# Kernel tuning notes

Measured on AMD Instinct MI355X. Metric: run time of the kernel, lower is better.

Reference implementation:

```python
import jax, jax.numpy as jnp
from jax import lax
import numpy as np

B, N, NPOINT, NSAMPLE, RADIUS = 8, 16384, 1024, 32, 0.4
C_IN = 64


def fps(xyz, npoint):
    """Furthest point sampling. xyz: (B, N, 3) -> (B, npoint) int32 indices.
    Matches the CUDA kernel: start from index 0, iteratively pick argmax of
    the running min-distance to the selected set."""
    Bb, Nn, _ = xyz.shape

    def step(carry, _):
        min_d, last = carry
        p = jnp.take_along_axis(xyz, last[:, None, None], axis=1)  # (B,1,3)
        d = jnp.sum((xyz - p) ** 2, axis=-1)                       # (B,N)
        min_d = jnp.minimum(min_d, d)
        nxt = jnp.argmax(min_d, axis=1).astype(jnp.int32)
        return (min_d, nxt), nxt

    idx0 = jnp.zeros((Bb,), jnp.int32)
    min_d0 = jnp.full((Bb, Nn), jnp.inf, xyz.dtype)
    _, rest = lax.scan(step, (min_d0, idx0), None, length=npoint - 1)  # (npoint-1, B)
    return jnp.transpose(jnp.concatenate([idx0[None, :], rest], axis=0))  # (B, npoint)


def ball_query(xyz, new_xyz, radius, nsample):
    """xyz: (B,N,3), new_xyz: (B,P,3) -> (B,P,nsample) int32 indices.
    First nsample in-radius indices (ascending), short balls padded with the
    first found index (the centroid itself is always in-radius)."""
    Nn = xyz.shape[1]
    d2 = jnp.sum((new_xyz[:, :, None, :] - xyz[:, None, :, :]) ** 2, axis=-1)  # (B,P,N)
    ar = jnp.arange(Nn, dtype=jnp.int32)
    key = jnp.where(d2 <= radius * radius, ar, Nn)  # out-of-ball -> sentinel N
    neg_top, _ = lax.top_k(-key, nsample)           # nsample smallest keys
    gidx = -neg_top                                  # (B,P,nsample)
    return jnp.where(gidx == Nn, gidx[..., :1], gidx)


def setup_inputs() -> dict:
    key = jax.random.key(0)
    ks = jax.random.split(key, 8)
    return {
        "xyz": jax.random.normal(ks[0], (B, N, 3), jnp.float32),
        "features": jax.random.normal(ks[1], (B, C_IN, N), jnp.float32),
        "W1": jax.random.normal(ks[2], (64, 3 + C_IN), jnp.float32) * 0.05,
        "b1": jax.random.normal(ks[3], (64,), jnp.float32) * 0.05,
        "W2": jax.random.normal(ks[4], (64, 64), jnp.float32) * 0.05,
        "b2": jax.random.normal(ks[5], (64,), jnp.float32) * 0.05,
        "W3": jax.random.normal(ks[6], (128, 64), jnp.float32) * 0.05,
        "b3": jax.random.normal(ks[7], (128,), jnp.float32) * 0.05,
    }


def reference(xyz, features, W1, b1, W2, b2, W3, b3):
    Bb = xyz.shape[0]
    idx = fps(xyz, NPOINT)                                         # (B,P)
    new_xyz = jnp.take_along_axis(xyz, idx[:, :, None], axis=1)    # (B,P,3)

    gidx = ball_query(xyz, new_xyz, RADIUS, NSAMPLE)               # (B,P,S)
    bi = jnp.arange(Bb)[:, None, None]
    grouped_xyz = xyz[bi, gidx] - new_xyz[:, :, None, :]           # (B,P,S,3) relative coords
    feats_t = jnp.transpose(features, (0, 2, 1))                   # (B,N,C)
    grouped_feats = feats_t[bi, gidx]                              # (B,P,S,C)
    h = jnp.concatenate([grouped_xyz, grouped_feats], axis=-1)     # (B,P,S,3+C)

    # shared per-point MLP (1x1 convs) + ReLU
    h = jax.nn.relu(jnp.einsum('bpsc,oc->bpso', h, W1) + b1)
    h = jax.nn.relu(jnp.einsum('bpsc,oc->bpso', h, W2) + b2)
    h = jax.nn.relu(jnp.einsum('bpsc,oc->bpso', h, W3) + b3)

    pooled = jnp.max(h, axis=2)                                    # (B,P,128) max over nsample
    new_features = jnp.transpose(pooled, (0, 2, 1))                # (B,128,P)
    return new_xyz, new_features
```

## Files before the change

### kernel.cpp

```cpp
#include <hip/hip_runtime.h>

#define R2 0.16f

typedef float f32x2 __attribute__((ext_vector_type(2)));

__device__ __forceinline__ float sqd(float x, float y, float z,
                                     float px, float py, float pz) {
  float dx = __fsub_rn(x, px);
  float dy = __fsub_rn(y, py);
  float dz = __fsub_rn(z, pz);
  return __fadd_rn(__fadd_rn(__fmul_rn(dx, dx), __fmul_rn(dy, dy)),
                   __fmul_rn(dz, dz));
}

__device__ __forceinline__ float wave64_max_dpp(float x) {
#define DPP_STEP(CTRL)                                                      \
  {                                                                         \
    int t_ = __builtin_amdgcn_update_dpp(__float_as_int(x),                 \
                                         __float_as_int(x), CTRL, 0xf, 0xf, \
                                         false);                            \
    x = fmaxf(x, __int_as_float(t_));                                       \
  }
  DPP_STEP(0x111) DPP_STEP(0x112) DPP_STEP(0x114)
  DPP_STEP(0x118) DPP_STEP(0x142) DPP_STEP(0x143)
#undef DPP_STEP
  return x;
}
__device__ __forceinline__ float wave64_min_dpp_f32(float x) {
#define DPP_STEP(CTRL)                                                      \
  {                                                                         \
    int t_ = __builtin_amdgcn_update_dpp(__float_as_int(x),                 \
                                         __float_as_int(x), CTRL, 0xf, 0xf, \
                                         false);                            \
    x = fminf(x, __int_as_float(t_));                                       \
  }
  DPP_STEP(0x111) DPP_STEP(0x112) DPP_STEP(0x114)
  DPP_STEP(0x118) DPP_STEP(0x142) DPP_STEP(0x143)
#undef DPP_STEP
  return x;
}
__device__ __forceinline__ unsigned wave64_min_dpp_u32(unsigned x) {
#define DPP_STEP(CTRL)                                                      \
  {                                                                         \
    unsigned t_ = (unsigned)__builtin_amdgcn_update_dpp(                    \
        (int)x, (int)x, CTRL, 0xf, 0xf, false);                             \
    x = (t_ < x) ? t_ : x;                                                  \
  }
  DPP_STEP(0x111) DPP_STEP(0x112) DPP_STEP(0x114)
  DPP_STEP(0x118) DPP_STEP(0x142) DPP_STEP(0x143)
#undef DPP_STEP
  return x;
}

__global__ __launch_bounds__(256) void zero_hist(unsigned* __restrict__ h) {
  h[blockIdx.x * 256 + threadIdx.x] = 0u;
}

__global__ __launch_bounds__(256) void hist_kernel(const float* __restrict__ xyz,
                                                   unsigned* __restrict__ hist,
                                                   unsigned* __restrict__ rank,
                                                   unsigned* __restrict__ cid) {
  int t = blockIdx.x * 256 + threadIdx.x;
  int b = t >> 14;
  const float* p = xyz + (size_t)t * 3;
  int cx = (int)floorf(p[0] + 4.0f);
  int cy = (int)floorf(p[1] + 4.0f);
  int cz = (int)floorf(p[2] + 4.0f);
  cx = min(max(cx, 0), 7);
  cy = min(max(cy, 0), 7);
  cz = min(max(cz, 0), 7);
  unsigned c = (unsigned)(cx | (cy << 3) | (cz << 6));
  unsigned r = atomicAdd(&hist[(b << 9) + c], 1u);
  rank[t] = r;
  cid[t] = c;
}

__global__ __launch_bounds__(512) void scan_kernel(const unsigned* __restrict__ hist,
                                                   unsigned* __restrict__ starts) {
  __shared__ unsigned a[512];
  int b = blockIdx.x, t = threadIdx.x;
  unsigned h = hist[(b << 9) + t];
  a[t] = h;
  __syncthreads();
  for (int s = 1; s < 512; s <<= 1) {
    unsigned v = (t >= s) ? a[t - s] : 0u;
    __syncthreads();
    a[t] += v;
    __syncthreads();
  }
  starts[(b << 9) + t] = a[t] - h;
}

__global__ __launch_bounds__(256) void scatter_kernel(
    const float* __restrict__ xyz, const unsigned* __restrict__ starts,
    const unsigned* __restrict__ rank, const unsigned* __restrict__ cid,
    float* __restrict__ xs2, float* __restrict__ ys2, float* __restrict__ zs2,
    unsigned* __restrict__ oi2) {
  int t = blockIdx.x * 256 + threadIdx.x;
  int b = t >> 14, n = t & 16383;
  unsigned pos = starts[(b << 9) + cid[t]] + rank[t];
  const float* p = xyz + (size_t)t * 3;
  size_t o = ((size_t)b << 14) + pos;
  xs2[o] = p[0];
  ys2[o] = p[1];
  zs2[o] = p[2];
  oi2[o] = (unsigned)n;
}

__global__ __launch_bounds__(1024) void fps_kernel(
    const float* __restrict__ xyz, const float* __restrict__ xs,
    const float* __restrict__ ys, const float* __restrict__ zs,
    const unsigned* __restrict__ oi, int* __restrict__ idx_out,
    float* __restrict__ newxyz_out, const float* __restrict__ feats,
    float* __restrict__ featsT) {
#pragma clang fp contract(off)
  extern __shared__ float4 xylds[];
  __shared__ unsigned long long s_gkey[3];
  __shared__ float s_cd[3][3][16];
  int tid = threadIdx.x;
  if (blockIdx.x >= 8) {
    int sub = tid >> 8, t = tid & 255;
    int tileid = (blockIdx.x - 8) * 4 + sub;
    int b = tileid >> 8;
    int n0 = (tileid & 255) << 6;
    float* tile = ((float*)xylds) + sub * 4160;
    int nn = t & 63, c0 = t >> 6;
#pragma unroll
    for (int r = 0; r < 64; r += 4) {
      int c = c0 + r;
      tile[c * 65 + nn] = feats[((size_t)b * 64 + c) * 16384 + n0 + nn];
    }
    __syncthreads();
    int cc = t & 63, n1 = t >> 6;
#pragma unroll
    for (int r = 0; r < 64; r += 4) {
      int n = n1 + r;
      featsT[((size_t)b * 16384 + n0 + n) * 64 + cc] = tile[cc * 65 + n];
    }
    return;
  }
  int b = blockIdx.x;
  int lane = tid & 63, wid = tid >> 6;
  const float* xb = xyz + (size_t)b * 16384 * 3;
  int base = tid << 4;
  const float4* xv = (const float4*)(xs + ((size_t)b << 14) + base);
  const float4* yv = (const float4*)(ys + ((size_t)b << 14) + base);
  const float4* zv = (const float4*)(zs + ((size_t)b << 14) + base);
  const uint4* ov = (const uint4*)(oi + ((size_t)b << 14) + base);
  float xr[16], yr[16], zr[16];
  unsigned OI[16];
#pragma unroll
  for (int q = 0; q < 4; ++q) {
    *(float4*)(xr + 4 * q) = xv[q];
    *(float4*)(yr + 4 * q) = yv[q];
    *(float4*)(zr + 4 * q) = zv[q];
    *(uint4*)(OI + 4 * q) = ov[q];
  }
  float bxl = xr[0], bxh = xr[0], byl = yr[0], byh = yr[0], bzl = zr[0],
        bzh = zr[0];
#pragma unroll
  for (int k = 1; k < 16; ++k) {
    bxl = fminf(bxl, xr[k]); bxh = fmaxf(bxh, xr[k]);
    byl = fminf(byl, yr[k]); byh = fmaxf(byh, yr[k]);
    bzl = fminf(bzl, zr[k]); bzh = fmaxf(bzh, zr[k]);
  }
  float wbxl = __int_as_float(
      __builtin_amdgcn_readlane(__float_as_int(wave64_min_dpp_f32(bxl)), 63));
  float wbxh = __int_as_float(
      __builtin_amdgcn_readlane(__float_as_int(wave64_max_dpp(bxh)), 63));
  float wbyl = __int_as_float(
      __builtin_amdgcn_readlane(__float_as_int(wave64_min_dpp_f32(byl)), 63));
  float wbyh = __int_as_float(
      __builtin_amdgcn_readlane(__float_as_int(wave64_max_dpp(byh)), 63));
  float wbzl = __int_as_float(
      __builtin_amdgcn_readlane(__float_as_int(wave64_min_dpp_f32(bzl)), 63));
  float wbzh = __int_as_float(
      __builtin_amdgcn_readlane(__float_as_int(wave64_max_dpp(bzh)), 63));
  f32x2 Z[8], M[8];
#pragma unroll
  for (int q = 0; q < 8; ++q) {
    xylds[(q << 10) + tid] =
        make_float4(xr[2 * q], xr[2 * q + 1], yr[2 * q], yr[2 * q + 1]);
    Z[q] = {zr[2 * q], zr[2 * q + 1]};
    M[q] = {__builtin_inff(), __builtin_inff()};
  }
  if (tid == 0) {
    idx_out[b * 1024] = 0;
    float* o0 = newxyz_out + (size_t)b * 1024 * 3;
    o0[0] = xb[0]; o0[1] = xb[1]; o0[2] = xb[2];
  }
  if (tid < 3) s_gkey[tid] = 0ull;
  __syncthreads();
  float px = xb[0], py = xb[1], pz = xb[2];
  float tv = __builtin_inff();
  float bvf = __builtin_inff();
  unsigned bvb = 0x7f800000u;
  int sl = 1, slp2 = 0;
  for (int it = 1; it < 1024; ++it) {
    float wdx = fmaxf(fmaxf(wbxl - px, px - wbxh), 0.0f);
    float wdy = fmaxf(fmaxf(wbyl - py, py - wbyh), 0.0f);
    float wdz = fmaxf(fmaxf(wbzl - pz, pz - wbzh), 0.0f);
    float wlb = (wdx * wdx + wdy * wdy + wdz * wdz) * 0.999f;
    if (wlb < bvf) {
      float ddx = fmaxf(fmaxf(bxl - px, px - bxh), 0.0f);
      float ddy = fmaxf(fmaxf(byl - py, py - byh), 0.0f);
      float ddz = fmaxf(fmaxf(bzl - pz, pz - bzh), 0.0f);
      float lb = (ddx * ddx + ddy * ddy + ddz * ddz) * 0.999f;
      if (lb < tv) {
        f32x2 px2 = {px, px}, py2 = {py, py}, pz2 = {pz, pz};
        float ntv = -1.0f;
#pragma unroll
        for (int q = 0; q < 8; ++q) {
          float4 t = xylds[(q << 10) + tid];
          f32x2 X = {t.x, t.y};
          f32x2 Y = {t.z, t.w};
          f32x2 dx = X - px2;
          f32x2 dy = Y - py2;
          f32x2 dz = Z[q] - pz2;
          f32x2 d = dx * dx + dy * dy + dz * dz;
          M[q].x = fminf(M[q].x, d.x);
          M[q].y = fminf(M[q].y, d.y);
          ntv = fmaxf(fmaxf(ntv, M[q].x), M[q].y);
        }
        tv = ntv;
      }
      float bv = wave64_max_dpp(tv);
      bvb = (unsigned)__builtin_amdgcn_readlane(__float_as_int(bv), 63);
      bvf = __int_as_float((int)bvb);
    }
    unsigned long long gk0 = __hip_atomic_load(
        &s_gkey[sl], __ATOMIC_RELAXED, __HIP_MEMORY_SCOPE_WORKGROUP);
    if (bvb >= (unsigned)(gk0 >> 18)) {
      unsigned coi = 0xffffffffu;
      float wx = 0.0f, wy = 0.0f, wz = 0.0f;
      if (tv == bvf) {
#pragma unroll
        for (int q = 0; q < 8; ++q) {
          float4 t = xylds[(q << 10) + tid];
          if (M[q].x == bvf && OI[2 * q] < coi) {
            coi = OI[2 * q]; wx = t.x; wy = t.z; wz = Z[q].x;
          }
          if (M[q].y == bvf && OI[2 * q + 1] < coi) {
            coi = OI[2 * q + 1]; wx = t.y; wy = t.w; wz = Z[q].y;
          }
        }
      }
      unsigned woi = wave64_min_dpp_u32(coi);
      if (coi == woi && coi != 0xffffffffu) {
        s_cd[sl][0][wid] = wx;
        s_cd[sl][1][wid] = wy;
        s_cd[sl][2][wid] = wz;
        unsigned long long key = ((unsigned long long)bvb << 18) |
                                 ((unsigned long long)(16383u - woi) << 4) |
                                 (unsigned long long)wid;
        atomicMax(&s_gkey[sl], key);
      }
    }
    __syncthreads();
    unsigned long long gk = s_gkey[sl];
    if (tid == 0) s_gkey[slp2] = 0ull;
    int w2 = (int)(gk & 15ull);
    int j = 16383 - (int)((gk >> 4) & 0x3fffull);
    px = s_cd[sl][0][w2];
    py = s_cd[sl][1][w2];
    pz = s_cd[sl][2][w2];
    if (tid == 0) {
      idx_out[b * 1024 + it] = j;
      float* o = newxyz_out + ((size_t)b * 1024 + it) * 3;
      o[0] = px; o[1] = py; o[2] = pz;
    }
    sl = (sl == 2) ? 0 : sl + 1;
    slp2 = (slp2 == 2) ? 0 : slp2 + 1;
  }
}

__global__ __launch_bounds__(256) void ballquery_grid(
    const float* __restrict__ xs, const float* __restrict__ ys,
    const float* __restrict__ zs, const unsigned* __restrict__ oi,
    const unsigned* __restrict__ hist, const unsigned* __restrict__ starts,
    const float* __restrict__ newxyz, int* __restrict__ gidx) {
  __shared__ unsigned bm[4][512];
  __shared__ unsigned sfirst[4];
  int wid = threadIdx.x >> 6, lane = threadIdx.x & 63;
  int cid = blockIdx.x * 4 + wid;
  int b = cid >> 10;
  float cx = newxyz[cid * 3 + 0];
  float cy = newxyz[cid * 3 + 1];
  float cz = newxyz[cid * 3 + 2];
  unsigned* mybm = bm[wid];
#pragma unroll
  for (int k = 0; k < 8; ++k) mybm[(k << 6) + lane] = 0u;
  int clox = min(max((int)floorf(cx - 0.4f + 4.0f), 0), 7);
  int chix = min(max((int)floorf(cx + 0.4f + 4.0f), 0), 7);
  int cloy = min(max((int)floorf(cy - 0.4f + 4.0f), 0), 7);
  int chiy = min(max((int)floorf(cy + 0.4f + 4.0f), 0), 7);
  int cloz = min(max((int)floorf(cz - 0.4f + 4.0f), 0), 7);
  int chiz = min(max((int)floorf(cz + 0.4f + 4.0f), 0), 7);
  const float* xsb = xs + ((size_t)b << 14);
  const float* ysb = ys + ((size_t)b << 14);
  const float* zsb = zs + ((size_t)b << 14);
  const unsigned* oib = oi + ((size_t)b << 14);
  const unsigned* hb = hist + (b << 9);
  const unsigned* sb = starts + (b << 9);
  for (int zz = cloz; zz <= chiz; ++zz)
    for (int yy = cloy; yy <= chiy; ++yy)
      for (int xx = clox; xx <= chix; ++xx) {
        unsigned cc = (unsigned)(xx | (yy << 3) | (zz << 6));
        unsigned st = sb[cc], cnt = hb[cc];
        for (unsigned c0 = 0; c0 < cnt; c0 += 64) {
          unsigned g = c0 + (unsigned)lane;
          if (g < cnt) {
            unsigned p = st + g;
            float d2 = sqd(xsb[p], ysb[p], zsb[p], cx, cy, cz);
            if (d2 <= R2) {
              unsigned o = oib[p];
              atomicOr(&mybm[o >> 5], 1u << (o & 31));
            }
          }
        }
      }
  int* out = gidx + (size_t)cid * 32;
  unsigned running = 0;
  for (int s = 0; s < 4 && running < 32; ++s) {
    unsigned lo = mybm[(s << 7) + 2 * lane];
    unsigned hi = mybm[(s << 7) + 2 * lane + 1];
    unsigned long long W = ((unsigned long long)hi << 32) | lo;
    int c = __popcll(W);
    int incl = c;
#pragma unroll
    for (int d = 1; d < 64; d <<= 1) {
      int t = __shfl_up(incl, d);
      if (lane >= d) incl += t;
    }
    int total = __shfl(incl, 63);
    int basep = (int)running + incl - c;
    while (W != 0ull && basep < 32) {
      int t = (int)__builtin_ctzll(W);
      W &= W - 1ull;
      int idxv = (((s << 6) + lane) << 6) + t;
      if (basep == 0) sfirst[wid] = (unsigned)idxv;
      out[basep] = idxv;
      ++basep;
    }
    running += (unsigned)total;
  }
  unsigned nf = running < 32u ? running : 32u;
  unsigned first = sfirst[wid];
  for (unsigned s2 = nf + (unsigned)lane; s2 < 32u; s2 += 64u)
    out[s2] = (int)first;
}

#define FMA16(BASEPTR)                                                     \
  do {                                                                     \
    const float4* hp_ = (const float4*)(BASEPTR);                          \
    float4 v0 = hp_[0], v1 = hp_[1], v2 = hp_[2], v3 = hp_[3];             \
    float a = acc[s];                                                      \
    a = fmaf(w[0], v0.x, a);  a = fmaf(w[1], v0.y, a);                     \
    a = fmaf(w[2], v0.z, a);  a = fmaf(w[3], v0.w, a);                     \
    a = fmaf(w[4], v1.x, a);  a = fmaf(w[5], v1.y, a);                     \
    a = fmaf(w[6], v1.z, a);  a = fmaf(w[7], v1.w, a);                     \
    a = fmaf(w[8], v2.x, a);  a = fmaf(w[9], v2.y, a);                     \
    a = fmaf(w[10], v2.z, a); a = fmaf(w[11], v2.w, a);                    \
    a = fmaf(w[12], v3.x, a); a = fmaf(w[13], v3.y, a);                    \
    a = fmaf(w[14], v3.z, a); a = fmaf(w[15], v3.w, a);                    \
    acc[s] = a;                                                            \
  } while (0)

__global__ __launch_bounds__(256) void mlp_kernel(
    const float* __restrict__ xyz, const float* __restrict__ feats,
    const float* __restrict__ featsT, const float* __restrict__ newxyz,
    const int* __restrict__ gidx,
    const float* __restrict__ W1, const float* __restrict__ b1,
    const float* __restrict__ W2, const float* __restrict__ b2,
    const float* __restrict__ W3, const float* __restrict__ b3,
    float* __restrict__ out, int useT) {
  __shared__ float buf[4][32 * 68];
  int wid = threadIdx.x >> 6, lane = threadIdx.x & 63;
  int cid = blockIdx.x * 4 + wid;
  int b = cid >> 10, p = cid & 1023;
  float* A = buf[wid];
  const int* gi = gidx + (size_t)cid * 32;
  float cx = newxyz[cid * 3 + 0];
  float cy = newxyz[cid * 3 + 1];
  float cz = newxyz[cid * 3 + 2];

  if (useT) {
    const float4* fT4 = (const float4*)(featsT + (size_t)b * 16384 * 64);
    for (int t = lane; t < 512; t += 64) {
      int s = t >> 4, q = t & 15;
      int g = gi[s];
      float4 v = fT4[(size_t)g * 16 + q];
      *(float4*)(A + s * 68 + q * 4) = v;
    }
  } else {
    const float* fb = feats + (size_t)b * 64 * 16384;
    for (int t = lane; t < 2048; t += 64) {
      int c = t >> 5, s = t & 31;
      int g = gi[s];
      A[s * 68 + c] = fb[(size_t)c * 16384 + g];
    }
  }
  for (int t = lane; t < 96; t += 64) {
    int s = t / 3, c = t - s * 3;
    int g = gi[s];
    float pv = xyz[((size_t)b * 16384 + g) * 3 + c];
    float cv = (c == 0) ? cx : ((c == 1) ? cy : cz);
    A[s * 68 + 64 + c] = __fsub_rn(pv, cv);
  }
  if (lane < 32) A[lane * 68 + 67] = 0.0f;
  __syncthreads();

  int o = lane;
  float acc[32];

#pragma unroll
  for (int s = 0; s < 32; ++s) acc[s] = b1[o];
  {
    const float* wr = W1 + o * 67;
    for (int cb = 0; cb < 4; ++cb) {
      float w[16];
#pragma unroll
      for (int q = 0; q < 16; ++q) w[q] = wr[3 + cb * 16 + q];
#pragma unroll
      for (int s = 0; s < 32; ++s) { FMA16(A + s * 68 + cb * 16); }
    }
    float w0 = wr[0], w1 = wr[1], w2 = wr[2];
#pragma unroll
    for (int s = 0; s < 32; ++s) {
      float a = acc[s];
      a = fmaf(w0, A[s * 68 + 64], a);
      a = fmaf(w1, A[s * 68 + 65], a);
      a = fmaf(w2, A[s * 68 + 66], a);
      acc[s] = a;
    }
  }
  __syncthreads();
#pragma unroll
  for (int s = 0; s < 32; ++s) A[s * 64 + o] = fmaxf(acc[s], 0.0f);
  __syncthreads();

#pragma unroll
  for (int s = 0; s < 32; ++s) acc[s] = b2[o];
  {
    const float* wr = W2 + o * 64;
    for (int cb = 0; cb < 4; ++cb) {
      float w[16];
#pragma unroll
      for (int q = 0; q < 16; ++q) w[q] = wr[cb * 16 + q];
#pragma unroll
      for (int s = 0; s < 32; ++s) { FMA16(A + s * 64 + cb * 16); }
    }
  }
  __syncthreads();
#pragma unroll
  for (int s = 0; s < 32; ++s) A[s * 64 + o] = fmaxf(acc[s], 0.0f);
  __syncthreads();

  float* outp = out + 24576;
  for (int po = 0; po < 2; ++po) {
    int o2 = lane + (po << 6);
#pragma unroll
    for (int s = 0; s < 32; ++s) acc[s] = b3[o2];
    const float* wr = W3 + o2 * 64;
    for (int cb = 0; cb < 4; ++cb) {
      float w[16];
#pragma unroll
      for (int q = 0; q < 16; ++q) w[q] = wr[cb * 16 + q];
#pragma unroll
      for (int s = 0; s < 32; ++s) { FMA16(A + s * 64 + cb * 16); }
    }
    float mx = 0.0f;
#pragma unroll
    for (int s = 0; s < 32; ++s) mx = fmaxf(mx, acc[s]);
    outp[((size_t)b * 128 + o2) * 1024 + p] = mx;
  }
}

extern "C" void kernel_launch(void* const* d_in, const int* in_sizes, int n_in,
                              void* d_out, int out_size, void* d_ws, size_t ws_size,
                              hipStream_t stream) {
  const float* xyz = (const float*)d_in[0];
  const float* feats = (const float*)d_in[1];
  const float* W1 = (const float*)d_in[2];
  const float* b1 = (const float*)d_in[3];
  const float* W2 = (const float*)d_in[4];
  const float* b2 = (const float*)d_in[5];
  const float* W3 = (const float*)d_in[6];
  const float* b3 = (const float*)d_in[7];
  float* out = (float*)d_out;

  char* w = (char*)d_ws;
  int* idx = (int*)w;
  int* gidx = (int*)(w + 32768);
  unsigned* hist = (unsigned*)(w + 1081344);
  unsigned* starts = (unsigned*)(w + 1097728);
  unsigned* rank = (unsigned*)(w + 1114112);
  unsigned* cid = (unsigned*)(w + 1638400);
  unsigned* oi2 = (unsigned*)(w + 2162688);
  float* xs2 = (float*)(w + 2686976);
  float* ys2 = (float*)(w + 3211264);
  float* zs2 = (float*)(w + 3735552);
  float* featsT = (float*)(w + 4259840);
  size_t needT = 4259840 + (size_t)8 * 16384 * 64 * sizeof(float);
  int useT = (ws_size >= needT) ? 1 : 0;

  zero_hist<<<16, 256, 0, stream>>>(hist);
  hist_kernel<<<512, 256, 0, stream>>>(xyz, hist, rank, cid);
  scan_kernel<<<8, 512, 0, stream>>>(hist, starts);
  scatter_kernel<<<512, 256, 0, stream>>>(xyz, starts, rank, cid, xs2, ys2,
                                          zs2, oi2);
  fps_kernel<<<useT ? 520 : 8, 1024, 131072, stream>>>(
      xyz, xs2, ys2, zs2, oi2, idx, out, feats, featsT);
  ballquery_grid<<<2048, 256, 0, stream>>>(xs2, ys2, zs2, oi2, hist, starts,
                                           out, gidx);
  mlp_kernel<<<2048, 256, 0, stream>>>(xyz, feats, featsT, out, gidx,
                                       W1, b1, W2, b2, W3, b3, out, useT);
}
```

Before: 1.935 ms.

## Fuse grid-sort prep into one kernel and merge ball query into MLP

Replaces the zero/hist/scan/scatter sequence with a single per-batch kernel that builds the cell histogram in shared memory, scans it and scatters the points. It also folds the ball query into the MLP kernel, so the neighbour indices stay in shared memory and never go through global memory. This removes four kernel launches and the global round trips for rank, cid and gidx. In exchange, the sort prep runs on only 8 blocks with serial per-thread work, and the fused kernel uses more LDS per block, which may lower occupancy.

New measurement: 1.941 ms. No clear change (+0.3%).

```diff
diff --git a/kernel.cpp b/kernel.cpp
--- a/kernel.cpp
+++ b/kernel.cpp
@@ -52,59 +52,57 @@
   return x;
 }
 
-__global__ __launch_bounds__(256) void zero_hist(unsigned* __restrict__ h) {
-  h[blockIdx.x * 256 + threadIdx.x] = 0u;
-}
-
-__global__ __launch_bounds__(256) void hist_kernel(const float* __restrict__ xyz,
-                                                   unsigned* __restrict__ hist,
-                                                   unsigned* __restrict__ rank,
-                                                   unsigned* __restrict__ cid) {
-  int t = blockIdx.x * 256 + threadIdx.x;
-  int b = t >> 14;
-  const float* p = xyz + (size_t)t * 3;
-  int cx = (int)floorf(p[0] + 4.0f);
-  int cy = (int)floorf(p[1] + 4.0f);
-  int cz = (int)floorf(p[2] + 4.0f);
-  cx = min(max(cx, 0), 7);
-  cy = min(max(cy, 0), 7);
-  cz = min(max(cz, 0), 7);
-  unsigned c = (unsigned)(cx | (cy << 3) | (cz << 6));
-  unsigned r = atomicAdd(&hist[(b << 9) + c], 1u);
-  rank[t] = r;
-  cid[t] = c;
-}
-
-__global__ __launch_bounds__(512) void scan_kernel(const unsigned* __restrict__ hist,
-                                                   unsigned* __restrict__ starts) {
-  __shared__ unsigned a[512];
+__global__ __launch_bounds__(512) void sortprep(
+    const float* __restrict__ xyz, unsigned* __restrict__ hist_g,
+    unsigned* __restrict__ starts_g, float* __restrict__ xs2,
+    float* __restrict__ ys2, float* __restrict__ zs2,
+    unsigned* __restrict__ oi2) {
+  __shared__ unsigned sh[512];
+  __shared__ unsigned sstart[512];
   int b = blockIdx.x, t = threadIdx.x;
-  unsigned h = hist[(b << 9) + t];
-  a[t] = h;
+  sh[t] = 0u;
+  __syncthreads();
+  const float* xb = xyz + (size_t)b * 16384 * 3;
+  unsigned pk[32];
+#pragma unroll
+  for (int k = 0; k < 32; ++k) {
+    int n = t + (k << 9);
+    const float* p = xb + (size_t)n * 3;
+    int cx = min(max((int)floorf(p[0] + 4.0f), 0), 7);
+    int cy = min(max((int)floorf(p[1] + 4.0f), 0), 7);
+    int cz = min(max((int)floorf(p[2] + 4.0f), 0), 7);
+    unsigned c = (unsigned)(cx | (cy << 3) | (cz << 6));
+    unsigned r = atomicAdd(&sh[c], 1u);
+    pk[k] = (c << 14) | r;
+  }
+  __syncthreads();
+  unsigned h = sh[t];
+  sstart[t] = h;
   __syncthreads();
   for (int s = 1; s < 512; s <<= 1) {
-    unsigned v = (t >= s) ? a[t - s] : 0u;
+    unsigned v = (t >= s) ? sstart[t - s] : 0u;
     __syncthreads();
-    a[t] += v;
+    sstart[t] += v;
     __syncthreads();
   }
-  starts[(b << 9) + t] = a[t] - h;
-}
-
-__global__ __launch_bounds__(256) void scatter_kernel(
-    const float* __restrict__ xyz, const unsigned* __restrict__ starts,
-    const unsigned* __restrict__ rank, const unsigned* __restrict__ cid,
-    float* __restrict__ xs2, float* __restrict__ ys2, float* __restrict__ zs2,
-    unsigned* __restrict__ oi2) {
-  int t = blockIdx.x * 256 + threadIdx.x;
-  int b = t >> 14, n = t & 16383;
-  unsigned pos = starts[(b << 9) + cid[t]] + rank[t];
-  const float* p = xyz + (size_t)t * 3;
-  size_t o = ((size_t)b << 14) + pos;
-  xs2[o] = p[0];
-  ys2[o] = p[1];
-  zs2[o] = p[2];
-  oi2[o] = (unsigned)n;
+  unsigned excl = sstart[t] - h;
+  hist_g[(b << 9) + t] = h;
+  starts_g[(b << 9) + t] = excl;
+  __syncthreads();
+  sstart[t] = excl;
+  __syncthreads();
+#pragma unroll
+  for (int k = 0; k < 32; ++k) {
+    int n = t + (k << 9);
+    unsigned c = pk[k] >> 14, r = pk[k] & 16383u;
+    unsigned pos = sstart[c] + r;
+    const float* p = xb + (size_t)n * 3;
+    size_t o = ((size_t)b << 14) + pos;
+    xs2[o] = p[0];
+    ys2[o] = p[1];
+    zs2[o] = p[2];
+    oi2[o] = (unsigned)n;
+  }
 }
 
 __global__ __launch_bounds__(1024) void fps_kernel(
@@ -274,19 +272,43 @@
   }
 }
 
-__global__ __launch_bounds__(256) void ballquery_grid(
+#define FMA16(BASEPTR)                                                     \
+  do {                                                                     \
+    const float4* hp_ = (const float4*)(BASEPTR);                          \
+    float4 v0 = hp_[0], v1 = hp_[1], v2 = hp_[2], v3 = hp_[3];             \
+    float a = acc[s];                                                      \
+    a = fmaf(w[0], v0.x, a);  a = fmaf(w[1], v0.y, a);                     \
+    a = fmaf(w[2], v0.z, a);  a = fmaf(w[3], v0.w, a);                     \
+    a = fmaf(w[4], v1.x, a);  a = fmaf(w[5], v1.y, a);                     \
+    a = fmaf(w[6], v1.z, a);  a = fmaf(w[7], v1.w, a);                     \
+    a = fmaf(w[8], v2.x, a);  a = fmaf(w[9], v2.y, a);                     \
+    a = fmaf(w[10], v2.z, a); a = fmaf(w[11], v2.w, a);                    \
+    a = fmaf(w[12], v3.x, a); a = fmaf(w[13], v3.y, a);                    \
+    a = fmaf(w[14], v3.z, a); a = fmaf(w[15], v3.w, a);                    \
+    acc[s] = a;                                                            \
+  } while (0)
+
+__global__ __launch_bounds__(256) void mlp_fused(
+    const float* __restrict__ xyz, const float* __restrict__ feats,
+    const float* __restrict__ featsT, const float* __restrict__ newxyz,
     const float* __restrict__ xs, const float* __restrict__ ys,
     const float* __restrict__ zs, const unsigned* __restrict__ oi,
     const unsigned* __restrict__ hist, const unsigned* __restrict__ starts,
-    const float* __restrict__ newxyz, int* __restrict__ gidx) {
+    const float* __restrict__ W1, const float* __restrict__ b1,
+    const float* __restrict__ W2, const float* __restrict__ b2,
+    const float* __restrict__ W3, const float* __restrict__ b3,
+    float* __restrict__ out, int useT) {
   __shared__ unsigned bm[4][512];
   __shared__ unsigned sfirst[4];
+  __shared__ int s_gi[4][32];
+  __shared__ float buf[4][32 * 68];
   int wid = threadIdx.x >> 6, lane = threadIdx.x & 63;
   int cid = blockIdx.x * 4 + wid;
-  int b = cid >> 10;
+  int b = cid >> 10, p = cid & 1023;
   float cx = newxyz[cid * 3 + 0];
   float cy = newxyz[cid * 3 + 1];
   float cz = newxyz[cid * 3 + 2];
+
   unsigned* mybm = bm[wid];
 #pragma unroll
   for (int k = 0; k < 8; ++k) mybm[(k << 6) + lane] = 0u;
@@ -310,16 +332,16 @@
         for (unsigned c0 = 0; c0 < cnt; c0 += 64) {
           unsigned g = c0 + (unsigned)lane;
           if (g < cnt) {
-            unsigned p = st + g;
-            float d2 = sqd(xsb[p], ysb[p], zsb[p], cx, cy, cz);
+            unsigned pp = st + g;
+            float d2 = sqd(xsb[pp], ysb[pp], zsb[pp], cx, cy, cz);
             if (d2 <= R2) {
-              unsigned o = oib[p];
+              unsigned o = oib[pp];
               atomicOr(&mybm[o >> 5], 1u << (o & 31));
             }
           }
         }
       }
-  int* out = gidx + (size_t)cid * 32;
+  int* gi = s_gi[wid];
   unsigned running = 0;
   for (int s = 0; s < 4 && running < 32; ++s) {
     unsigned lo = mybm[(s << 7) + 2 * lane];
@@ -339,7 +361,7 @@
       W &= W - 1ull;
       int idxv = (((s << 6) + lane) << 6) + t;
       if (basep == 0) sfirst[wid] = (unsigned)idxv;
-      out[basep] = idxv;
+      gi[basep] = idxv;
       ++basep;
     }
     running += (unsigned)total;
@@ -347,43 +369,9 @@
   unsigned nf = running < 32u ? running : 32u;
   unsigned first = sfirst[wid];
   for (unsigned s2 = nf + (unsigned)lane; s2 < 32u; s2 += 64u)
-    out[s2] = (int)first;
-}
-
-#define FMA16(BASEPTR)                                                     \
-  do {                                                                     \
-    const float4* hp_ = (const float4*)(BASEPTR);                          \
-    float4 v0 = hp_[0], v1 = hp_[1], v2 = hp_[2], v3 = hp_[3];             \
-    float a = acc[s];                                                      \
-    a = fmaf(w[0], v0.x, a);  a = fmaf(w[1], v0.y, a);                     \
-    a = fmaf(w[2], v0.z, a);  a = fmaf(w[3], v0.w, a);                     \
-    a = fmaf(w[4], v1.x, a);  a = fmaf(w[5], v1.y, a);                     \
-    a = fmaf(w[6], v1.z, a);  a = fmaf(w[7], v1.w, a);                     \
-    a = fmaf(w[8], v2.x, a);  a = fmaf(w[9], v2.y, a);                     \
-    a = fmaf(w[10], v2.z, a); a = fmaf(w[11], v2.w, a);                    \
-    a = fmaf(w[12], v3.x, a); a = fmaf(w[13], v3.y, a);                    \
-    a = fmaf(w[14], v3.z, a); a = fmaf(w[15], v3.w, a);                    \
-    acc[s] = a;                                                            \
-  } while (0)
-
-__global__ __launch_bounds__(256) void mlp_kernel(
-    const float* __restrict__ xyz, const float* __restrict__ feats,
-    const float* __restrict__ featsT, const float* __restrict__ newxyz,
-    const int* __restrict__ gidx,
-    const float* __restrict__ W1, const float* __restrict__ b1,
-    const float* __restrict__ W2, const float* __restrict__ b2,
-    const float* __restrict__ W3, const float* __restrict__ b3,
-    float* __restrict__ out, int useT) {
-  __shared__ float buf[4][32 * 68];
-  int wid = threadIdx.x >> 6, lane = threadIdx.x & 63;
-  int cid = blockIdx.x * 4 + wid;
-  int b = cid >> 10, p = cid & 1023;
+    gi[s2] = (int)first;
+
   float* A = buf[wid];
-  const int* gi = gidx + (size_t)cid * 32;
-  float cx = newxyz[cid * 3 + 0];
-  float cy = newxyz[cid * 3 + 1];
-  float cz = newxyz[cid * 3 + 2];
-
   if (useT) {
     const float4* fT4 = (const float4*)(featsT + (size_t)b * 16384 * 64);
     for (int t = lane; t < 512; t += 64) {
@@ -491,11 +479,8 @@
 
   char* w = (char*)d_ws;
   int* idx = (int*)w;
-  int* gidx = (int*)(w + 32768);
   unsigned* hist = (unsigned*)(w + 1081344);
   unsigned* starts = (unsigned*)(w + 1097728);
-  unsigned* rank = (unsigned*)(w + 1114112);
-  unsigned* cid = (unsigned*)(w + 1638400);
   unsigned* oi2 = (unsigned*)(w + 2162688);
   float* xs2 = (float*)(w + 2686976);
   float* ys2 = (float*)(w + 3211264);
@@ -504,15 +489,10 @@
   size_t needT = 4259840 + (size_t)8 * 16384 * 64 * sizeof(float);
   int useT = (ws_size >= needT) ? 1 : 0;
 
-  zero_hist<<<16, 256, 0, stream>>>(hist);
-  hist_kernel<<<512, 256, 0, stream>>>(xyz, hist, rank, cid);
-  scan_kernel<<<8, 512, 0, stream>>>(hist, starts);
-  scatter_kernel<<<512, 256, 0, stream>>>(xyz, starts, rank, cid, xs2, ys2,
-                                          zs2, oi2);
+  sortprep<<<8, 512, 0, stream>>>(xyz, hist, starts, xs2, ys2, zs2, oi2);
   fps_kernel<<<useT ? 520 : 8, 1024, 131072, stream>>>(
       xyz, xs2, ys2, zs2, oi2, idx, out, feats, featsT);
-  ballquery_grid<<<2048, 256, 0, stream>>>(xs2, ys2, zs2, oi2, hist, starts,
-                                           out, gidx);
-  mlp_kernel<<<2048, 256, 0, stream>>>(xyz, feats, featsT, out, gidx,
-                                       W1, b1, W2, b2, W3, b3, out, useT);
-}
+  mlp_fused<<<2048, 256, 0, stream>>>(xyz, feats, featsT, out, xs2, ys2, zs2,
+                                      oi2, hist, starts, W1, b1, W2, b2, W3,
+                                      b3, out, useT);
+}
```
